# Performance work log

Hardware: AMD Instinct MI355X
Metric: run time of the kernel (lower is better)

Reference implementation:

```python
import jax, jax.numpy as jnp
import numpy as np

TEMPERATURE = 1.0
EPS = 1e-8
B, D, N, K = 2048, 32, 8192, 30


def setup_inputs() -> dict:
    key = jax.random.key(0)
    k1, k2, k3 = jax.random.split(key, 3)
    z_current = jax.random.normal(k1, (B, D), dtype=jnp.float32)
    pre_knn_indices = jax.random.randint(k2, (N, K), 0, N, dtype=jnp.int64 if jax.config.jax_enable_x64 else jnp.int32)
    sample_indices = jax.random.randint(k3, (B,), 0, N, dtype=jnp.int64 if jax.config.jax_enable_x64 else jnp.int32)
    return {"z_current": z_current, "pre_knn_indices": pre_knn_indices, "sample_indices": sample_indices}


def reference(z_current, pre_knn_indices, sample_indices):
    b = z_current.shape[0]
    eye = jnp.eye(b, dtype=bool)
    # pairwise Euclidean distance via gram trick: (B,B), avoids (B,B,D) intermediate
    sq = jnp.sum(z_current * z_current, axis=-1)
    d2 = jnp.maximum(sq[:, None] + sq[None, :] - 2.0 * (z_current @ z_current.T), 0.0)
    d2_safe = jnp.where(eye, 1.0, d2)  # avoid sqrt(0) on diagonal (masked below anyway)
    dist = jnp.sqrt(d2_safe)
    sim = jnp.where(eye, -jnp.inf, -dist / TEMPERATURE)
    soft_neighbors = jax.nn.softmax(sim, axis=1)  # (B,B)
    # neighbor mask: j is kept iff global id of j is in pre-kNN set of i, and j != i
    knn = pre_knn_indices[sample_indices]  # (B,K) global ids of i's pre-neighbors
    in_set = (knn[:, :, None] == sample_indices[None, None, :]).any(axis=1)  # (B,B)
    mask = in_set & ~eye
    s = jnp.sum(soft_neighbors * mask, axis=1)  # (B,)
    valid = mask.any(axis=1)
    count = valid.sum()
    loss_i = -jnp.log(s + EPS)
    total = jnp.sum(jnp.where(valid, loss_i, 0.0))
    return jnp.where(count > 0, total / count, jnp.float32(0.0))
```

## Files before the change

### kernel.cpp

```cpp
#include <hip/hip_runtime.h>
#include <math.h>

#define Bsz 2048
#define Ddim 32
#define Nsz 8192
#define Kk 30
#define TPB 256
#define ROWS 4
#define NBLK (Bsz / ROWS)
#define JCH (Bsz / TPB)
#define NW (Nsz / 32)

__global__ __launch_bounds__(TPB, 2) void softnp_main(
    const float* __restrict__ z,
    const int*   __restrict__ pre_knn,
    const int*   __restrict__ samp,
    float*       __restrict__ acc,
    float*       __restrict__ out)
{
    __shared__ unsigned bits4[NW][ROWS];
    __shared__ int      sampsh[Bsz];
    __shared__ float    zish[ROWS * Ddim];
    __shared__ float    rden[4][ROWS], rnum[4][ROWS];
    __shared__ int      rcnt[4][ROWS];

    const int t  = threadIdx.x;
    const int i0 = blockIdx.x * ROWS;

    #pragma unroll
    for (int c = 0; c < ROWS; ++c)
        ((unsigned*)bits4)[t + c * TPB] = 0u;
    #pragma unroll
    for (int c = 0; c < JCH; ++c)
        sampsh[t + c * TPB] = samp[t + c * TPB];
    if (t < ROWS * Ddim) zish[t] = z[(size_t)i0 * Ddim + t];
    __syncthreads();

    if (t < ROWS * 32) {
        const int r = t >> 5, k = t & 31;
        if (k < Kk) {
            const int id = pre_knn[(size_t)sampsh[i0 + r] * Kk + k];
            atomicOr(&bits4[id >> 5][r], 1u << (id & 31));
        }
    }
    __syncthreads();

    float4 zi[ROWS][Ddim / 4];
    const float4* z4 = (const float4*)zish;
    #pragma unroll
    for (int r = 0; r < ROWS; ++r)
        #pragma unroll
        for (int d = 0; d < Ddim / 4; ++d)
            zi[r][d] = z4[r * (Ddim / 4) + d];

    float den[ROWS] = {0.f, 0.f, 0.f, 0.f};
    float num[ROWS] = {0.f, 0.f, 0.f, 0.f};
    int   cnt[ROWS] = {0, 0, 0, 0};

    const float4* zg = (const float4*)z;
    int j = t;
    float4 cur[8];
    #pragma unroll
    for (int d = 0; d < 8; ++d) cur[d] = zg[(size_t)j * 8 + d];

    #pragma unroll
    for (int c = 0; c < JCH; ++c) {
        float4 nxt[8];
        const int jn = j + TPB;
        if (c + 1 < JCH) {
            #pragma unroll
            for (int d = 0; d < 8; ++d) nxt[d] = zg[(size_t)jn * 8 + d];
        }

        float d2[ROWS] = {0.f, 0.f, 0.f, 0.f};
        #pragma unroll
        for (int d = 0; d < 8; ++d) {
            const float4 v = cur[d];
            #pragma unroll
            for (int r = 0; r < ROWS; ++r) {
                const float dx = zi[r][d].x - v.x;
                const float dy = zi[r][d].y - v.y;
                const float dz_ = zi[r][d].z - v.z;
                const float dw = zi[r][d].w - v.w;
                d2[r] += dx * dx + dy * dy + dz_ * dz_ + dw * dw;
            }
        }

        const int   sj = sampsh[j];
        const uint4 bw = ((const uint4*)bits4)[sj >> 5];
        const unsigned bsel[4] = {bw.x, bw.y, bw.z, bw.w};
        #pragma unroll
        for (int r = 0; r < ROWS; ++r) {
            const bool diag = (j == i0 + r);
            const float e = diag ? 0.f : __expf(-sqrtf(d2[r]));
            den[r] += e;
            if (!diag && ((bsel[r] >> (sj & 31)) & 1u)) { num[r] += e; cnt[r]++; }
        }

        if (c + 1 < JCH) {
            #pragma unroll
            for (int d = 0; d < 8; ++d) cur[d] = nxt[d];
        }
        j = jn;
    }

    const int lane = t & 63, wv = t >> 6;
    #pragma unroll
    for (int r = 0; r < ROWS; ++r) {
        #pragma unroll
        for (int off = 32; off > 0; off >>= 1) {
            den[r] += __shfl_xor(den[r], off, 64);
            num[r] += __shfl_xor(num[r], off, 64);
            cnt[r] += __shfl_xor(cnt[r], off, 64);
        }
    }
    if (lane == 0) {
        #pragma unroll
        for (int r = 0; r < ROWS; ++r) {
            rden[wv][r] = den[r]; rnum[wv][r] = num[r]; rcnt[wv][r] = cnt[r];
        }
    }
    __syncthreads();

    if (t < ROWS) {
        float D = 0.f, Nm = 0.f; int C = 0;
        #pragma unroll
        for (int w = 0; w < 4; ++w) { D += rden[w][t]; Nm += rnum[w][t]; C += rcnt[w][t]; }
        if (C > 0) {
            atomicAdd(&acc[0], -__logf(Nm / D + 1e-8f));
            atomicAdd(&acc[1], 1.0f);
        }
    }
    __syncthreads();

    if (t == 0) {
        __threadfence();
        const unsigned prev = atomicAdd((unsigned*)(acc + 2), 1u);
        if (prev == (unsigned)(gridDim.x - 1)) {
            __threadfence();
            const float a0 = atomicAdd(&acc[0], 0.0f);
            const float a1 = atomicAdd(&acc[1], 0.0f);
            out[0] = (a1 > 0.f) ? a0 / a1 : 0.f;
        }
    }
}

extern "C" void kernel_launch(void* const* d_in, const int* in_sizes, int n_in,
                              void* d_out, int out_size, void* d_ws, size_t ws_size,
                              hipStream_t stream)
{
    const float* z       = (const float*)d_in[0];
    const int*   pre_knn = (const int*)d_in[1];
    const int*   samp    = (const int*)d_in[2];
    float*       out     = (float*)d_out;
    float*       acc     = (float*)d_ws;

    hipMemsetAsync(acc, 0, 3 * sizeof(float), stream);

    softnp_main<<<dim3(NBLK), dim3(TPB), 0, stream>>>(z, pre_knn, samp, acc, out);
}
```

Measured before the change: 94.09 us.

## Split column range across two blocks, use gram-trick distances, reduce in a second kernel

Each row group now gets two blocks, each covering half of the j columns, which doubles the grid for better CU coverage. Squared distances are computed from dot products and precomputed squared norms instead of elementwise differences. Per-row partial denominators and numerators go to workspace, and a small second kernel does the final log-loss reduction. This replaces the global atomics, the completion counter and the memset. The trade-offs are an extra launch, possible cancellation error from the gram trick, and validity now being judged by Nm > 0 instead of a neighbor count.

```diff
diff --git a/kernel.cpp b/kernel.cpp
--- a/kernel.cpp
+++ b/kernel.cpp
@@ -7,43 +7,48 @@
 #define Kk 30
 #define TPB 256
 #define ROWS 4
-#define NBLK (Bsz / ROWS)
-#define JCH (Bsz / TPB)
+#define JSL 2
+#define JTILE (Bsz / JSL)
+#define JCH (JTILE / TPB)
+#define NBLK ((Bsz / ROWS) * JSL)
 #define NW (Nsz / 32)
 
 __global__ __launch_bounds__(TPB, 2) void softnp_main(
     const float* __restrict__ z,
     const int*   __restrict__ pre_knn,
     const int*   __restrict__ samp,
-    float*       __restrict__ acc,
-    float*       __restrict__ out)
+    float*       __restrict__ wsden,
+    float*       __restrict__ wsnum)
 {
     __shared__ unsigned bits4[NW][ROWS];
-    __shared__ int      sampsh[Bsz];
+    __shared__ int      sampsh[JTILE];
     __shared__ float    zish[ROWS * Ddim];
+    __shared__ int      rowsi[ROWS];
     __shared__ float    rden[4][ROWS], rnum[4][ROWS];
-    __shared__ int      rcnt[4][ROWS];
 
     const int t  = threadIdx.x;
-    const int i0 = blockIdx.x * ROWS;
+    const int rg = blockIdx.x >> 1;
+    const int sl = blockIdx.x & 1;
+    const int i0 = rg * ROWS;
+    const int jb = sl * JTILE;
 
     #pragma unroll
-    for (int c = 0; c < ROWS; ++c)
+    for (int c = 0; c < (NW * ROWS) / TPB; ++c)
         ((unsigned*)bits4)[t + c * TPB] = 0u;
     #pragma unroll
     for (int c = 0; c < JCH; ++c)
-        sampsh[t + c * TPB] = samp[t + c * TPB];
+        sampsh[t + c * TPB] = samp[jb + t + c * TPB];
     if (t < ROWS * Ddim) zish[t] = z[(size_t)i0 * Ddim + t];
+    if (t < ROWS) rowsi[t] = samp[i0 + t];
     __syncthreads();
 
     if (t < ROWS * 32) {
         const int r = t >> 5, k = t & 31;
         if (k < Kk) {
-            const int id = pre_knn[(size_t)sampsh[i0 + r] * Kk + k];
+            const int id = pre_knn[(size_t)rowsi[r] * Kk + k];
             atomicOr(&bits4[id >> 5][r], 1u << (id & 31));
         }
     }
-    __syncthreads();
 
     float4 zi[ROWS][Ddim / 4];
     const float4* z4 = (const float4*)zish;
@@ -53,12 +58,23 @@
         for (int d = 0; d < Ddim / 4; ++d)
             zi[r][d] = z4[r * (Ddim / 4) + d];
 
+    float si2[ROWS];
+    #pragma unroll
+    for (int r = 0; r < ROWS; ++r) {
+        float s = 0.f;
+        #pragma unroll
+        for (int d = 0; d < Ddim / 4; ++d)
+            s += zi[r][d].x * zi[r][d].x + zi[r][d].y * zi[r][d].y
+               + zi[r][d].z * zi[r][d].z + zi[r][d].w * zi[r][d].w;
+        si2[r] = s;
+    }
+    __syncthreads();
+
     float den[ROWS] = {0.f, 0.f, 0.f, 0.f};
     float num[ROWS] = {0.f, 0.f, 0.f, 0.f};
-    int   cnt[ROWS] = {0, 0, 0, 0};
 
     const float4* zg = (const float4*)z;
-    int j = t;
+    int j = jb + t;
     float4 cur[8];
     #pragma unroll
     for (int d = 0; d < 8; ++d) cur[d] = zg[(size_t)j * 8 + d];
@@ -66,42 +82,40 @@
     #pragma unroll
     for (int c = 0; c < JCH; ++c) {
         float4 nxt[8];
-        const int jn = j + TPB;
         if (c + 1 < JCH) {
             #pragma unroll
-            for (int d = 0; d < 8; ++d) nxt[d] = zg[(size_t)jn * 8 + d];
+            for (int d = 0; d < 8; ++d) nxt[d] = zg[(size_t)(j + TPB) * 8 + d];
         }
 
-        float d2[ROWS] = {0.f, 0.f, 0.f, 0.f};
+        float dot[ROWS] = {0.f, 0.f, 0.f, 0.f};
+        float sj2 = 0.f;
         #pragma unroll
         for (int d = 0; d < 8; ++d) {
             const float4 v = cur[d];
+            sj2 += v.x * v.x + v.y * v.y + v.z * v.z + v.w * v.w;
             #pragma unroll
-            for (int r = 0; r < ROWS; ++r) {
-                const float dx = zi[r][d].x - v.x;
-                const float dy = zi[r][d].y - v.y;
-                const float dz_ = zi[r][d].z - v.z;
-                const float dw = zi[r][d].w - v.w;
-                d2[r] += dx * dx + dy * dy + dz_ * dz_ + dw * dw;
-            }
+            for (int r = 0; r < ROWS; ++r)
+                dot[r] += zi[r][d].x * v.x + zi[r][d].y * v.y
+                        + zi[r][d].z * v.z + zi[r][d].w * v.w;
         }
 
-        const int   sj = sampsh[j];
+        const int   sj = sampsh[t + c * TPB];
         const uint4 bw = ((const uint4*)bits4)[sj >> 5];
         const unsigned bsel[4] = {bw.x, bw.y, bw.z, bw.w};
         #pragma unroll
         for (int r = 0; r < ROWS; ++r) {
+            const float d2 = fmaxf(si2[r] + sj2 - 2.f * dot[r], 0.f);
             const bool diag = (j == i0 + r);
-            const float e = diag ? 0.f : __expf(-sqrtf(d2[r]));
+            const float e = diag ? 0.f : __expf(-sqrtf(d2));
             den[r] += e;
-            if (!diag && ((bsel[r] >> (sj & 31)) & 1u)) { num[r] += e; cnt[r]++; }
+            if (!diag && ((bsel[r] >> (sj & 31)) & 1u)) num[r] += e;
         }
 
         if (c + 1 < JCH) {
             #pragma unroll
             for (int d = 0; d < 8; ++d) cur[d] = nxt[d];
         }
-        j = jn;
+        j += TPB;
     }
 
     const int lane = t & 63, wv = t >> 6;
@@ -111,37 +125,53 @@
         for (int off = 32; off > 0; off >>= 1) {
             den[r] += __shfl_xor(den[r], off, 64);
             num[r] += __shfl_xor(num[r], off, 64);
-            cnt[r] += __shfl_xor(cnt[r], off, 64);
         }
     }
     if (lane == 0) {
         #pragma unroll
-        for (int r = 0; r < ROWS; ++r) {
-            rden[wv][r] = den[r]; rnum[wv][r] = num[r]; rcnt[wv][r] = cnt[r];
-        }
+        for (int r = 0; r < ROWS; ++r) { rden[wv][r] = den[r]; rnum[wv][r] = num[r]; }
     }
     __syncthreads();
 
     if (t < ROWS) {
-        float D = 0.f, Nm = 0.f; int C = 0;
+        float D = 0.f, Nm = 0.f;
         #pragma unroll
-        for (int w = 0; w < 4; ++w) { D += rden[w][t]; Nm += rnum[w][t]; C += rcnt[w][t]; }
-        if (C > 0) {
-            atomicAdd(&acc[0], -__logf(Nm / D + 1e-8f));
-            atomicAdd(&acc[1], 1.0f);
+        for (int w = 0; w < 4; ++w) { D += rden[w][t]; Nm += rnum[w][t]; }
+        wsden[sl * Bsz + i0 + t] = D;
+        wsnum[sl * Bsz + i0 + t] = Nm;
+    }
+}
+
+__global__ __launch_bounds__(TPB) void softnp_final(
+    const float* __restrict__ wsden,
+    const float* __restrict__ wsnum,
+    float*       __restrict__ out)
+{
+    __shared__ float rl[4], rc[4];
+    const int t = threadIdx.x;
+    float loss = 0.f, vcnt = 0.f;
+    #pragma unroll
+    for (int c = 0; c < Bsz / TPB; ++c) {
+        const int r = t + c * TPB;
+        const float D  = wsden[r] + wsden[Bsz + r];
+        const float Nm = wsnum[r] + wsnum[Bsz + r];
+        if (Nm > 0.f) {
+            loss -= __logf(Nm / D + 1e-8f);
+            vcnt += 1.f;
         }
     }
+    #pragma unroll
+    for (int off = 32; off > 0; off >>= 1) {
+        loss += __shfl_xor(loss, off, 64);
+        vcnt += __shfl_xor(vcnt, off, 64);
+    }
+    const int lane = t & 63, wv = t >> 6;
+    if (lane == 0) { rl[wv] = loss; rc[wv] = vcnt; }
     __syncthreads();
-
     if (t == 0) {
-        __threadfence();
-        const unsigned prev = atomicAdd((unsigned*)(acc + 2), 1u);
-        if (prev == (unsigned)(gridDim.x - 1)) {
-            __threadfence();
-            const float a0 = atomicAdd(&acc[0], 0.0f);
-            const float a1 = atomicAdd(&acc[1], 0.0f);
-            out[0] = (a1 > 0.f) ? a0 / a1 : 0.f;
-        }
+        const float L = rl[0] + rl[1] + rl[2] + rl[3];
+        const float C = rc[0] + rc[1] + rc[2] + rc[3];
+        out[0] = (C > 0.f) ? L / C : 0.f;
     }
 }
 
@@ -153,9 +183,9 @@
     const int*   pre_knn = (const int*)d_in[1];
     const int*   samp    = (const int*)d_in[2];
     float*       out     = (float*)d_out;
-    float*       acc     = (float*)d_ws;
+    float*       wsden   = (float*)d_ws;
+    float*       wsnum   = wsden + JSL * Bsz;
 
-    hipMemsetAsync(acc, 0, 3 * sizeof(float), stream);
-
-    softnp_main<<<dim3(NBLK), dim3(TPB), 0, stream>>>(z, pre_knn, samp, acc, out);
+    softnp_main<<<dim3(NBLK), dim3(TPB), 0, stream>>>(z, pre_knn, samp, wsden, wsnum);
+    softnp_final<<<dim3(1), dim3(TPB), 0, stream>>>(wsden, wsnum, out);
 }
```

Measured after the change: 84.52 us. 1.11x faster.
